# Kernel tuning notes

Hardware: AMD Instinct MI355X
Metric: run time of the kernel (lower is better)

Reference implementation:

```python
import jax, jax.numpy as jnp
import numpy as np

B, T, C, H = 4, 2048, 2048, 16
D = C // H  # head dim = 128


def setup_inputs() -> dict:
    key = jax.random.key(0)
    k1, k2, k3, k4 = jax.random.split(key, 4)
    x = jax.random.normal(k1, (B, T, C), dtype=jnp.float32)
    # per-token key mask; force token 0 valid so no causal row is fully masked
    tok_mask = jax.random.randint(k2, (B, T), 0, 2).astype(bool).at[:, 0].set(True)
    s = 1.0 / np.sqrt(C).astype(np.float32)
    W_qkv = jax.random.normal(k3, (C, 3 * C), dtype=jnp.float32) * s
    W_proj = jax.random.normal(k4, (C, C), dtype=jnp.float32) * s
    return {"x": x, "tok_mask": tok_mask, "W_qkv": W_qkv, "W_proj": W_proj}


def reference(x, tok_mask, W_qkv, W_proj):
    Bx, Tx, Cx = x.shape
    qkv = x @ W_qkv                              # [B,T,3C]
    q, k, v = jnp.split(qkv, 3, axis=-1)
    q = q.reshape(Bx, Tx, H, D)
    k = k.reshape(Bx, Tx, H, D)
    v = v.reshape(Bx, Tx, H, D)
    scale = 1.0 / np.sqrt(D).astype(np.float32)
    scores = jnp.einsum('bqhd,bkhd->bhqk', q, k) * scale  # [B,H,T,T]
    causal = jnp.tril(jnp.ones((Tx, Tx), dtype=bool))      # [T,T]
    # tok_mask broadcasts over the query dim (key mask), AND-ed with causal
    mask = tok_mask[:, None, :] & causal                   # [B,T,T]
    scores = jnp.where(mask[:, None, :, :], scores, -jnp.inf)
    attn = jax.nn.softmax(scores, axis=-1)                 # dropout p=0 -> identity
    y = jnp.einsum('bhqk,bkhd->bqhd', attn, v).reshape(Bx, Tx, Cx)
    return y @ W_proj
```

## Files before the change

### kernel.cpp

```cpp
#include <hip/hip_runtime.h>
#include <hip/hip_bf16.h>
#include <stdint.h>

typedef __bf16 bf16;
typedef __bf16 bf16x8 __attribute__((ext_vector_type(8)));
typedef float f32x4 __attribute__((ext_vector_type(4)));
typedef unsigned short u16;
typedef unsigned int u32;

constexpr int NB = 4;
constexpr int NT = 2048;
constexpr int NC = 2048;
constexpr int NH = 16;
constexpr int ND = 128;
constexpr int NC3 = 6144;

__device__ __forceinline__ void gload16(const void* g, void* l) {
  __builtin_amdgcn_global_load_lds((const __attribute__((address_space(1))) void*)g,
                                   (__attribute__((address_space(3))) void*)l, 16, 0, 0);
}

__device__ __forceinline__ u32 pack_bf16(float a, float b) {
  return (u32)__builtin_bit_cast(u16, (bf16)a) | ((u32)__builtin_bit_cast(u16, (bf16)b) << 16);
}

__global__ __launch_bounds__(256) void ingest_k(const float* __restrict__ raw, bf16* __restrict__ out, long n) {
  long i = ((long)blockIdx.x * 256 + threadIdx.x) * 8;
  if (i >= n) return;
  f32x4 a = *(const f32x4*)(raw + i), b = *(const f32x4*)(raw + i + 4);
  bf16x8 o;
  o[0] = (bf16)a[0]; o[1] = (bf16)a[1]; o[2] = (bf16)a[2]; o[3] = (bf16)a[3];
  o[4] = (bf16)b[0]; o[5] = (bf16)b[1]; o[6] = (bf16)b[2]; o[7] = (bf16)b[3];
  *(bf16x8*)(out + i) = o;
}

__global__ void mask_prep_k(const void* raw, int* out) {
  __shared__ int s_gt1, s_oddnz, s_allb, s_allf, s_allh;
  if (threadIdx.x == 0) { s_gt1 = 0; s_oddnz = 0; s_allb = 1; s_allf = 1; s_allh = 1; }
  __syncthreads();
  const unsigned int* mw = (const unsigned int*)raw;
  int gt1 = 0, oddnz = 0, allb = 1, allf = 1, allh = 1;
  for (int i = threadIdx.x; i < 2048; i += 256) {
    unsigned v = mw[i];
    if (v > 1u) gt1 = 1;
    if ((i & 1) && v) oddnz = 1;
#pragma unroll
    for (int bb = 0; bb < 4; ++bb) { unsigned by = (v >> (8*bb)) & 0xffu; if (by > 1u) allb = 0; }
    if (v != 0u && v != 0x3F800000u) allf = 0;
    unsigned lo = v & 0xffffu, hi = v >> 16;
    if ((lo != 0u && lo != 0x3F80u) || (hi != 0u && hi != 0x3F80u)) allh = 0;
  }
  if (gt1) atomicOr(&s_gt1, 1);
  if (oddnz) atomicOr(&s_oddnz, 1);
  if (!allb) atomicAnd(&s_allb, 0);
  if (!allf) atomicAnd(&s_allf, 0);
  if (!allh) atomicAnd(&s_allh, 0);
  __syncthreads();
  int mode;
  if (!s_gt1)       mode = s_oddnz ? 0 : 2;
  else if (s_allf)  mode = 3;
  else if (s_allb)  mode = 1;
  else if (s_allh)  mode = 4;
  else              mode = 0;
  for (int i = threadIdx.x; i < NB*NT; i += 256) {
    int v;
    if (mode == 0)      v = (((const int*)raw)[i] != 0);
    else if (mode == 1) v = (((const unsigned char*)raw)[i] != 0);
    else if (mode == 2) v = (((const long long*)raw)[i] != 0);
    else if (mode == 3) v = (((const unsigned int*)raw)[i] != 0);
    else                v = (((const unsigned short*)raw)[i] != 0);
    out[i] = v;
  }
}

__global__ __launch_bounds__(256) void transpose_f32_k(const float* __restrict__ in, bf16* __restrict__ out,
                                                       int in_rs, int out_rs) {
  __shared__ __align__(16) bf16 t[64][72];
  const int r0 = blockIdx.y << 6, c0 = blockIdx.x << 6;
  const int tid = threadIdx.x;
#pragma unroll
  for (int i = 0; i < 4; ++i) {
    int slot = i*256 + tid, row = slot >> 4, c4 = slot & 15;
    f32x4 v = *(const f32x4*)(in + (long)(r0 + row)*in_rs + c0 + c4*4);
#pragma unroll
    for (int e = 0; e < 4; ++e) t[c4*4 + e][row] = (bf16)v[e];
  }
  __syncthreads();
#pragma unroll
  for (int i = 0; i < 2; ++i) {
    int slot = i*256 + tid, row = slot >> 3, c8 = slot & 7;
    bf16x8 v = *(const bf16x8*)(&t[row][c8*8]);
    *(bf16x8*)(out + (long)(c0 + row)*out_rs + r0 + c8*8) = v;
  }
}

__global__ __launch_bounds__(256) void vtrans_k(const bf16* __restrict__ qkv, bf16* __restrict__ vt) {
  __shared__ __align__(16) bf16 t[64][72];
  const int tt = blockIdx.x, dh = blockIdx.y, bh = blockIdx.z;
  const int b = bh >> 4, h = bh & 15;
  const int tid = threadIdx.x;
  const bf16* src = qkv + (long)(b*NT + tt*64)*NC3 + (2*NC + h*ND + dh*64);
#pragma unroll
  for (int i = 0; i < 2; ++i) {
    int slot = i*256 + tid, row = slot >> 3, c8 = slot & 7;
    bf16x8 v = *(const bf16x8*)(src + (long)row*NC3 + c8*8);
#pragma unroll
    for (int e = 0; e < 8; ++e) t[c8*8 + e][row] = v[e];
  }
  __syncthreads();
  bf16* dst = vt + ((long)bh*ND + dh*64)*NT + tt*64;
#pragma unroll
  for (int i = 0; i < 2; ++i) {
    int slot = i*256 + tid, row = slot >> 3, c8 = slot & 7;
    bf16x8 v = *(const bf16x8*)(&t[row][c8*8]);
    *(bf16x8*)(dst + (long)row*NT + c8*8) = v;
  }
}

template <typename OT>
__global__ __launch_bounds__(512, 2) void gemm256_k(const bf16* __restrict__ A, const bf16* __restrict__ BT,
                                                    OT* __restrict__ Cout, int M, int N, int K, int nbx) {
  const int nwg = gridDim.x;
  const int bid = blockIdx.x;
  const int cpx = nwg >> 3;
  const int swz = (bid & 7) * cpx + (bid >> 3);
  const int bx = swz % nbx, by = swz / nbx;
  const long m0 = (long)by << 8, n0 = (long)bx << 8;

  const int tid = threadIdx.x, w = tid >> 6, l = tid & 63, g = l >> 4, r = l & 15;
  const int wm = w >> 2, wn = w & 3;

  __shared__ __align__(16) char As[2][32768];
  __shared__ __align__(16) char Bs[2][32768];

  long aoff[4], boff[4];
  int slo[4];
#pragma unroll
  for (int i = 0; i < 4; ++i) {
    int s = i*512 + tid, row = s >> 3, c = s & 7, cp = c ^ (row & 7);
    aoff[i] = (m0 + row)*(long)K + cp*8;
    boff[i] = (n0 + row)*(long)K + cp*8;
    slo[i] = (i*512 + w*64) << 4;
  }

  const f32x4 z4 = {0.f, 0.f, 0.f, 0.f};
  f32x4 acc[8][4];
#pragma unroll
  for (int i = 0; i < 8; ++i)
#pragma unroll
    for (int j = 0; j < 4; ++j) acc[i][j] = z4;

  const int nk = K >> 6;
#pragma unroll
  for (int i = 0; i < 4; ++i) {
    gload16(A + aoff[i], As[0] + slo[i]);
    gload16(BT + boff[i], Bs[0] + slo[i]);
  }
  __syncthreads();

  bf16x8 af[8], bfr[4];

  for (int t = 0; t < nk; ++t) {
    const int cur = t & 1;
    const char* Ac = As[cur];
    const char* Bc = Bs[cur];

#pragma unroll
    for (int mi = 0; mi < 4; ++mi)
#pragma unroll
      for (int kk = 0; kk < 2; ++kk) {
        int row = wm*128 + mi*16 + r;
        af[mi*2+kk] = *(const bf16x8*)(Ac + row*128 + (((kk*4 + g) ^ (row & 7)) << 4));
      }
#pragma unroll
    for (int ni = 0; ni < 2; ++ni)
#pragma unroll
      for (int kk = 0; kk < 2; ++kk) {
        int row = wn*64 + ni*16 + r;
        bfr[ni*2+kk] = *(const bf16x8*)(Bc + row*128 + (((kk*4 + g) ^ (row & 7)) << 4));
      }
    if (t + 1 < nk) {
      const long ko = (long)(t+1) << 6;
#pragma unroll
      for (int i = 0; i < 4; ++i) {
        gload16(A + aoff[i] + ko, As[cur^1] + slo[i]);
        gload16(BT + boff[i] + ko, Bs[cur^1] + slo[i]);
      }
    }
    __builtin_amdgcn_s_setprio(1);
#pragma unroll
    for (int mi = 0; mi < 4; ++mi)
#pragma unroll
      for (int ni = 0; ni < 2; ++ni)
#pragma unroll
        for (int kk = 0; kk < 2; ++kk)
          acc[mi][ni] = __builtin_amdgcn_mfma_f32_16x16x32_bf16(af[mi*2+kk], bfr[ni*2+kk], acc[mi][ni], 0, 0, 0);
    __builtin_amdgcn_s_setprio(0);
    __builtin_amdgcn_s_barrier();

#pragma unroll
    for (int mi = 0; mi < 4; ++mi)
#pragma unroll
      for (int kk = 0; kk < 2; ++kk) {
        int row = wm*128 + 64 + mi*16 + r;
        af[mi*2+kk] = *(const bf16x8*)(Ac + row*128 + (((kk*4 + g) ^ (row & 7)) << 4));
      }
    __builtin_amdgcn_s_setprio(1);
#pragma unroll
    for (int mi = 0; mi < 4; ++mi)
#pragma unroll
      for (int ni = 0; ni < 2; ++ni)
#pragma unroll
        for (int kk = 0; kk < 2; ++kk)
          acc[4+mi][ni] = __builtin_amdgcn_mfma_f32_16x16x32_bf16(af[mi*2+kk], bfr[ni*2+kk], acc[4+mi][ni], 0, 0, 0);
    __builtin_amdgcn_s_setprio(0);
    __builtin_amdgcn_s_barrier();

#pragma unroll
    for (int ni = 0; ni < 2; ++ni)
#pragma unroll
      for (int kk = 0; kk < 2; ++kk) {
        int row = wn*64 + 32 + ni*16 + r;
        bfr[ni*2+kk] = *(const bf16x8*)(Bc + row*128 + (((kk*4 + g) ^ (row & 7)) << 4));
      }
    __builtin_amdgcn_s_setprio(1);
#pragma unroll
    for (int mi = 0; mi < 4; ++mi)
#pragma unroll
      for (int ni = 0; ni < 2; ++ni)
#pragma unroll
        for (int kk = 0; kk < 2; ++kk)
          acc[4+mi][2+ni] = __builtin_amdgcn_mfma_f32_16x16x32_bf16(af[mi*2+kk], bfr[ni*2+kk], acc[4+mi][2+ni], 0, 0, 0);
    __builtin_amdgcn_s_setprio(0);
    __builtin_amdgcn_s_barrier();

#pragma unroll
    for (int mi = 0; mi < 4; ++mi)
#pragma unroll
      for (int kk = 0; kk < 2; ++kk) {
        int row = wm*128 + mi*16 + r;
        af[mi*2+kk] = *(const bf16x8*)(Ac + row*128 + (((kk*4 + g) ^ (row & 7)) << 4));
      }
    __builtin_amdgcn_s_setprio(1);
#pragma unroll
    for (int mi = 0; mi < 4; ++mi)
#pragma unroll
      for (int ni = 0; ni < 2; ++ni)
#pragma unroll
        for (int kk = 0; kk < 2; ++kk)
          acc[mi][2+ni] = __builtin_amdgcn_mfma_f32_16x16x32_bf16(af[mi*2+kk], bfr[ni*2+kk], acc[mi][2+ni], 0, 0, 0);
    __builtin_amdgcn_s_setprio(0);
    __syncthreads();
  }

#pragma unroll
  for (int mi = 0; mi < 8; ++mi)
#pragma unroll
    for (int ni = 0; ni < 4; ++ni)
#pragma unroll
      for (int j = 0; j < 4; ++j) {
        long mr = m0 + wm*128 + mi*16 + 4*g + j;
        long nc = n0 + wn*64 + ni*16 + r;
        Cout[mr*(long)N + nc] = (OT)acc[mi][ni][j];
      }
}

__global__ __launch_bounds__(256, 2) void attn_k(const bf16* __restrict__ qkv, const bf16* __restrict__ vt,
                                                 const int* __restrict__ mask, bf16* __restrict__ y) {
  const int qx = blockIdx.x, h = blockIdx.y, b = blockIdx.z;
  const int qb = (qx & 1) ? (15 - (qx >> 1)) : (qx >> 1);
  const int tid = threadIdx.x, w = tid >> 6, l = tid & 63, g = l >> 4, r = l & 15;
  const int q0 = qb << 7;
  const int bh = b*NH + h;
  const int ntiles = (qb << 1) + 2;
  const int qrowA = q0 + w*32 + r;
  const int qrowB = qrowA + 16;

  __shared__ __align__(16) char Klds[2][16384];
  __shared__ __align__(16) char Vlds[2][16384];
  __shared__ __align__(16) char Plds[8192];
  __shared__ char Mc[2048];
  char* Pl = Plds + (w << 11);

  for (int i = tid; i < q0 + 128; i += 256) Mc[i] = (char)(mask[b*NT + i] != 0);

  long koff[4], voff[4];
  int klo[4];
#pragma unroll
  for (int i = 0; i < 4; ++i) {
    int slot = i*256 + tid;
    int row = slot >> 4, c = slot & 15, cp = c ^ (row & 7);
    koff[i] = (long)row*NC3 + cp*8;
    klo[i] = (i*256 + w*64) << 4;
    int vrow = slot >> 3, vc = slot & 7, vcp = vc ^ (vrow & 7);
    voff[i] = (long)vrow*NT + vcp*8;
  }
  const bf16* kbase0 = qkv + (long)(b*NT)*NC3 + (NC + h*ND);
  const bf16* vbase0 = vt + (long)bh*ND*NT;

  bf16x8 qfA[4], qfB[4];
  {
    const bf16* qpA = qkv + (long)(b*NT + qrowA)*NC3 + h*ND + g*8;
    const bf16* qpB = qkv + (long)(b*NT + qrowB)*NC3 + h*ND + g*8;
#pragma unroll
    for (int dk = 0; dk < 4; ++dk) {
      qfA[dk] = *(const bf16x8*)(qpA + dk*32);
      qfB[dk] = *(const bf16x8*)(qpB + dk*32);
    }
  }

  const f32x4 z4 = {0.f, 0.f, 0.f, 0.f};
  f32x4 accA[8], accB[8];
#pragma unroll
  for (int i = 0; i < 8; ++i) { accA[i] = z4; accB[i] = z4; }
  float m_runA = 0.0f, l_runA = 0.0f;
  float m_runB = 0.0f, l_runB = 0.0f;

  const float SCL = 0.08838834764831845f * 1.4426950408889634f;

#pragma unroll
  for (int i = 0; i < 4; ++i) {
    gload16(kbase0 + koff[i], Klds[0] + klo[i]);
    gload16(vbase0 + voff[i], Vlds[0] + klo[i]);
  }
  __syncthreads();

  for (int kt = 0; kt < ntiles; ++kt) {
    const int cur = kt & 1;
    if (kt + 1 < ntiles) {
      const bf16* kb = kbase0 + (long)((kt+1)*64)*NC3;
      const bf16* vb = vbase0 + (kt+1)*64;
#pragma unroll
      for (int i = 0; i < 4; ++i) {
        gload16(kb + koff[i], Klds[cur^1] + klo[i]);
        gload16(vb + voff[i], Vlds[cur^1] + klo[i]);
      }
    }
    const char* Kl = Klds[cur];
    const char* Vl = Vlds[cur];
    const int key0 = kt*64;
    const bool actB = (key0 <= q0 + w*32 + 31);
    const bool actA = (key0 <= q0 + w*32 + 15);

    if (actB) {
      u32 mw_[4];
#pragma unroll
      for (int kc = 0; kc < 4; ++kc) mw_[kc] = *(const u32*)(Mc + key0 + kc*16 + 4*g);

      float tvA[4][4], tvB[4][4];
      __builtin_amdgcn_s_setprio(1);
#pragma unroll
      for (int kc = 0; kc < 4; ++kc) {
        const int krow = kc*16 + r;
        bf16x8 kf[4];
#pragma unroll
        for (int dk = 0; dk < 4; ++dk)
          kf[dk] = *(const bf16x8*)(Kl + krow*256 + (((dk*4 + g) ^ (krow & 7)) << 4));
        f32x4 sB = z4;
#pragma unroll
        for (int dk = 0; dk < 4; ++dk)
          sB = __builtin_amdgcn_mfma_f32_16x16x32_bf16(kf[dk], qfB[dk], sB, 0, 0, 0);
        f32x4 sA = z4;
        if (actA) {
#pragma unroll
          for (int dk = 0; dk < 4; ++dk)
            sA = __builtin_amdgcn_mfma_f32_16x16x32_bf16(kf[dk], qfA[dk], sA, 0, 0, 0);
        }
#pragma unroll
        for (int j = 0; j < 4; ++j) {
          const int key = key0 + kc*16 + 4*g + j;
          const bool km = ((mw_[kc] >> (8*j)) & 0xffu) != 0;
          tvB[kc][j] = (km && key <= qrowB) ? sB[j]*SCL : -3.0e38f;
          tvA[kc][j] = (km && key <= qrowA) ? sA[j]*SCL : -3.0e38f;
        }
      }
      __builtin_amdgcn_s_setprio(0);

      bf16x8 paA[2], paB[2];
      if (actA) {
        float tmax = -3.0e38f;
#pragma unroll
        for (int kc = 0; kc < 4; ++kc)
#pragma unroll
          for (int j = 0; j < 4; ++j) tmax = fmaxf(tmax, tvA[kc][j]);
        tmax = fmaxf(tmax, __shfl_xor(tmax, 16));
        tmax = fmaxf(tmax, __shfl_xor(tmax, 32));
        if (!__all(tmax <= m_runA + 8.0f)) {
          float mn = fmaxf(m_runA, tmax);
          float al = exp2f(m_runA - mn);
          m_runA = mn;
          l_runA *= al;
          float alj[4];
#pragma unroll
          for (int j = 0; j < 4; ++j) alj[j] = __shfl(al, 4*g + j);
#pragma unroll
          for (int d0 = 0; d0 < 8; ++d0)
#pragma unroll
            for (int j = 0; j < 4; ++j) accA[d0][j] *= alj[j];
        }
        float rs = 0.f;
#pragma unroll
        for (int kc = 0; kc < 4; ++kc) {
          float p0 = exp2f(tvA[kc][0] - m_runA), p1 = exp2f(tvA[kc][1] - m_runA);
          float p2 = exp2f(tvA[kc][2] - m_runA), p3 = exp2f(tvA[kc][3] - m_runA);
          rs += (p0 + p1) + (p2 + p3);
          const int off = (kc*32 + g*8) ^ ((r & 7) << 4);
          uint2 wv; wv.x = pack_bf16(p0, p1); wv.y = pack_bf16(p2, p3);
          *(uint2*)(Pl + r*128 + off) = wv;
        }
        rs += __shfl_xor(rs, 16);
        rs += __shfl_xor(rs, 32);
        l_runA += rs;
        asm volatile("s_waitcnt lgkmcnt(0)" ::: "memory");
        __builtin_amdgcn_sched_barrier(0);
#pragma unroll
        for (int kk = 0; kk < 2; ++kk)
          paA[kk] = *(const bf16x8*)(Pl + r*128 + ((kk*64 + g*16) ^ ((r & 7) << 4)));
        asm volatile("s_waitcnt lgkmcnt(0)" ::: "memory");
        __builtin_amdgcn_sched_barrier(0);
      }
      {
        float tmax = -3.0e38f;
#pragma unroll
        for (int kc = 0; kc < 4; ++kc)
#pragma unroll
          for (int j = 0; j < 4; ++j) tmax = fmaxf(tmax, tvB[kc][j]);
        tmax = fmaxf(tmax, __shfl_xor(tmax, 16));
        tmax = fmaxf(tmax, __shfl_xor(tmax, 32));
        if (!__all(tmax <= m_runB + 8.0f)) {
          float mn = fmaxf(m_runB, tmax);
          float al = exp2f(m_runB - mn);
          m_runB = mn;
          l_runB *= al;
          float alj[4];
#pragma unroll
          for (int j = 0; j < 4; ++j) alj[j] = __shfl(al, 4*g + j);
#pragma unroll
          for (int d0 = 0; d0 < 8; ++d0)
#pragma unroll
            for (int j = 0; j < 4; ++j) accB[d0][j] *= alj[j];
        }
        float rs = 0.f;
#pragma unroll
        for (int kc = 0; kc < 4; ++kc) {
          float p0 = exp2f(tvB[kc][0] - m_runB), p1 = exp2f(tvB[kc][1] - m_runB);
          float p2 = exp2f(tvB[kc][2] - m_runB), p3 = exp2f(tvB[kc][3] - m_runB);
          rs += (p0 + p1) + (p2 + p3);
          const int off = (kc*32 + g*8) ^ ((r & 7) << 4);
          uint2 wv; wv.x = pack_bf16(p0, p1); wv.y = pack_bf16(p2, p3);
          *(uint2*)(Pl + r*128 + off) = wv;
        }
        rs += __shfl_xor(rs, 16);
        rs += __shfl_xor(rs, 32);
        l_runB += rs;
        asm volatile("s_waitcnt lgkmcnt(0)" ::: "memory");
        __builtin_amdgcn_sched_barrier(0);
#pragma unroll
        for (int kk = 0; kk < 2; ++kk)
          paB[kk] = *(const bf16x8*)(Pl + r*128 + ((kk*64 + g*16) ^ ((r & 7) << 4)));
      }

      __builtin_amdgcn_s_setprio(1);
#pragma unroll
      for (int d0 = 0; d0 < 8; ++d0) {
        const int vrow = d0*16 + r;
#pragma unroll
        for (int kk = 0; kk < 2; ++kk) {
          bf16x8 vf = *(const bf16x8*)(Vl + vrow*128 + (((kk*4 + g) ^ (vrow & 7)) << 4));
          accB[d0] = __builtin_amdgcn_mfma_f32_16x16x32_bf16(paB[kk], vf, accB[d0], 0, 0, 0);
          if (actA) accA[d0] = __builtin_amdgcn_mfma_f32_16x16x32_bf16(paA[kk], vf, accA[d0], 0, 0, 0);
        }
      }
      __builtin_amdgcn_s_setprio(0);
    }
    __syncthreads();
  }

  {
    float lrA[4], lrB[4];
#pragma unroll
    for (int j = 0; j < 4; ++j) {
      lrA[j] = __shfl(l_runA, 4*g + j);
      lrB[j] = __shfl(l_runB, 4*g + j);
    }
#pragma unroll
    for (int d0 = 0; d0 < 8; ++d0)
#pragma unroll
      for (int j = 0; j < 4; ++j) {
        int qrA = q0 + w*32 + 4*g + j;
        y[(long)(b*NT + qrA)*NC + h*ND + d0*16 + r] = (bf16)(accA[d0][j] / lrA[j]);
        y[(long)(b*NT + qrA + 16)*NC + h*ND + d0*16 + r] = (bf16)(accB[d0][j] / lrB[j]);
      }
  }
}

extern "C" void kernel_launch(void* const* d_in, const int* in_sizes, int n_in,
                              void* d_out, int out_size, void* d_ws, size_t ws_size,
                              hipStream_t stream) {
  const float* xr     = (const float*)d_in[0];
  const void*  tok    = d_in[1];
  const float* wqkvr  = (const float*)d_in[2];
  const float* wprojr = (const float*)d_in[3];
  float* out = (float*)d_out;
  char* ws = (char*)d_ws;

  bf16* qkv    = (bf16*)(ws);
  bf16* yattn  = (bf16*)(ws + 100663296L);
  bf16* wT     = (bf16*)(ws + 134217728L);
  bf16* wpT    = (bf16*)(ws + 159383552L);
  bf16* xb     = (bf16*)(ws + 167772160L);
  bf16* vtb    = xb;
  int*  maskI  = (int*)(ws + 201326592L);

  mask_prep_k<<<1, 256, 0, stream>>>(tok, maskI);
  ingest_k<<<8192, 256, 0, stream>>>(xr, xb, 16777216L);
  transpose_f32_k<<<dim3(96, 32), 256, 0, stream>>>(wqkvr, wT, NC3, NC);
  transpose_f32_k<<<dim3(32, 32), 256, 0, stream>>>(wprojr, wpT, NC, NC);
  gemm256_k<bf16><<<768, 512, 0, stream>>>(xb, wT, qkv, 8192, 6144, 2048, 24);
  vtrans_k<<<dim3(32, 2, 64), 256, 0, stream>>>(qkv, vtb);
  attn_k<<<dim3(16, 16, 4), 256, 0, stream>>>(qkv, vtb, maskI, yattn);
  gemm256_k<float><<<256, 512, 0, stream>>>(yattn, wpT, out, 8192, 2048, 2048, 8);
}
```

Baseline: 548.3 us.

## Restructure gemm256 prefetch with per-wave LDS regions and explicit vmcnt waits

Remaps the global-to-LDS loads so each wave group fills the A/B rows it later reads, and splits the next-tile prefetch across the first two phases of the k-loop. Replaces the full __syncthreads at the end of each iteration with explicit s_waitcnt vmcnt counts plus s_barrier and sched_barrier, and peels the last iteration. The aim is to overlap global loads with MFMA work and avoid draining all outstanding memory ops every k-step. The hand-tuned vmcnt values must match the exact number of issued loads, so any compiler reordering or count mismatch could cause races.

```diff
diff --git a/kernel.cpp b/kernel.cpp
--- a/kernel.cpp
+++ b/kernel.cpp
@@ -117,6 +117,43 @@
   }
 }
 
+#define G256_READ_A(qm_) \
+  _Pragma("unroll") \
+  for (int mi = 0; mi < 4; ++mi) { \
+    _Pragma("unroll") \
+    for (int kk = 0; kk < 2; ++kk) { \
+      const int ri = (qm_)*64 + mi*16 + r; \
+      af[mi*2+kk] = *(const bf16x8*)(Ac + wm*16384 + ri*128 + (((kk*4 + g) ^ (ri & 7)) << 4)); \
+    } \
+  }
+#define G256_READ_B(qn_) \
+  _Pragma("unroll") \
+  for (int ni = 0; ni < 2; ++ni) { \
+    _Pragma("unroll") \
+    for (int kk = 0; kk < 2; ++kk) { \
+      const int ri = (qn_)*32 + ni*16 + r; \
+      bfr[ni*2+kk] = *(const bf16x8*)(Bc + wn*8192 + ri*128 + (((kk*4 + g) ^ (ri & 7)) << 4)); \
+    } \
+  }
+#define G256_MFMA(mb_, nb_) \
+  __builtin_amdgcn_s_setprio(1); \
+  _Pragma("unroll") \
+  for (int mi = 0; mi < 4; ++mi) \
+    _Pragma("unroll") \
+    for (int ni = 0; ni < 2; ++ni) \
+      _Pragma("unroll") \
+      for (int kk = 0; kk < 2; ++kk) \
+        acc[(mb_)+mi][(nb_)+ni] = __builtin_amdgcn_mfma_f32_16x16x32_bf16(af[mi*2+kk], bfr[ni*2+kk], acc[(mb_)+mi][(nb_)+ni], 0, 0, 0); \
+  __builtin_amdgcn_s_setprio(0);
+#define G256_EDGE(vm_) \
+  asm volatile("s_waitcnt vmcnt(" #vm_ ")" ::: "memory"); \
+  __builtin_amdgcn_s_barrier(); \
+  __builtin_amdgcn_sched_barrier(0);
+#define G256_EDGE_NOVM() \
+  asm volatile("" ::: "memory"); \
+  __builtin_amdgcn_s_barrier(); \
+  __builtin_amdgcn_sched_barrier(0);
+
 template <typename OT>
 __global__ __launch_bounds__(512, 2) void gemm256_k(const bf16* __restrict__ A, const bf16* __restrict__ BT,
                                                     OT* __restrict__ Cout, int M, int N, int K, int nbx) {
@@ -133,14 +170,18 @@
   __shared__ __align__(16) char As[2][32768];
   __shared__ __align__(16) char Bs[2][32768];
 
-  long aoff[4], boff[4];
-  int slo[4];
+  long aoff2[4], boff2[4];
+  int alds[4], blds[4];
 #pragma unroll
   for (int i = 0; i < 4; ++i) {
-    int s = i*512 + tid, row = s >> 3, c = s & 7, cp = c ^ (row & 7);
-    aoff[i] = (m0 + row)*(long)K + cp*8;
-    boff[i] = (n0 + row)*(long)K + cp*8;
-    slo[i] = (i*512 + w*64) << 4;
+    int s = i*256 + (tid & 255);
+    int ri = s >> 3, c = s & 7, cp = c ^ (ri & 7);
+    aoff2[i] = (m0 + wm*128 + ri) * (long)K + cp*8;
+    alds[i] = wm*16384 + ((i*256 + (w & 3)*64) << 4);
+    int s2 = i*128 + wm*64 + l;
+    int ri2 = s2 >> 3, c2 = s2 & 7, cp2 = c2 ^ (ri2 & 7);
+    boff2[i] = (n0 + wn*64 + ri2) * (long)K + cp2*8;
+    blds[i] = wn*8192 + ((i*128 + wm*64) << 4);
   }
 
   const f32x4 z4 = {0.f, 0.f, 0.f, 0.f};
@@ -151,106 +192,66 @@
     for (int j = 0; j < 4; ++j) acc[i][j] = z4;
 
   const int nk = K >> 6;
-#pragma unroll
-  for (int i = 0; i < 4; ++i) {
-    gload16(A + aoff[i], As[0] + slo[i]);
-    gload16(BT + boff[i], Bs[0] + slo[i]);
-  }
-  __syncthreads();
+  gload16(A + aoff2[0], As[0] + alds[0]);
+  gload16(A + aoff2[1], As[0] + alds[1]);
+  gload16(BT + boff2[0], Bs[0] + blds[0]);
+  gload16(BT + boff2[1], Bs[0] + blds[1]);
+  gload16(A + aoff2[2], As[0] + alds[2]);
+  gload16(A + aoff2[3], As[0] + alds[3]);
+  gload16(BT + boff2[2], Bs[0] + blds[2]);
+  gload16(BT + boff2[3], Bs[0] + blds[3]);
+  G256_EDGE(4);
 
   bf16x8 af[8], bfr[4];
 
-  for (int t = 0; t < nk; ++t) {
+  for (int t = 0; t < nk - 1; ++t) {
     const int cur = t & 1;
     const char* Ac = As[cur];
     const char* Bc = Bs[cur];
-
-#pragma unroll
-    for (int mi = 0; mi < 4; ++mi)
-#pragma unroll
-      for (int kk = 0; kk < 2; ++kk) {
-        int row = wm*128 + mi*16 + r;
-        af[mi*2+kk] = *(const bf16x8*)(Ac + row*128 + (((kk*4 + g) ^ (row & 7)) << 4));
-      }
-#pragma unroll
-    for (int ni = 0; ni < 2; ++ni)
-#pragma unroll
-      for (int kk = 0; kk < 2; ++kk) {
-        int row = wn*64 + ni*16 + r;
-        bfr[ni*2+kk] = *(const bf16x8*)(Bc + row*128 + (((kk*4 + g) ^ (row & 7)) << 4));
-      }
-    if (t + 1 < nk) {
-      const long ko = (long)(t+1) << 6;
-#pragma unroll
-      for (int i = 0; i < 4; ++i) {
-        gload16(A + aoff[i] + ko, As[cur^1] + slo[i]);
-        gload16(BT + boff[i] + ko, Bs[cur^1] + slo[i]);
-      }
-    }
-    __builtin_amdgcn_s_setprio(1);
-#pragma unroll
-    for (int mi = 0; mi < 4; ++mi)
-#pragma unroll
-      for (int ni = 0; ni < 2; ++ni)
-#pragma unroll
-        for (int kk = 0; kk < 2; ++kk)
-          acc[mi][ni] = __builtin_amdgcn_mfma_f32_16x16x32_bf16(af[mi*2+kk], bfr[ni*2+kk], acc[mi][ni], 0, 0, 0);
-    __builtin_amdgcn_s_setprio(0);
-    __builtin_amdgcn_s_barrier();
-
-#pragma unroll
-    for (int mi = 0; mi < 4; ++mi)
-#pragma unroll
-      for (int kk = 0; kk < 2; ++kk) {
-        int row = wm*128 + 64 + mi*16 + r;
-        af[mi*2+kk] = *(const bf16x8*)(Ac + row*128 + (((kk*4 + g) ^ (row & 7)) << 4));
-      }
-    __builtin_amdgcn_s_setprio(1);
-#pragma unroll
-    for (int mi = 0; mi < 4; ++mi)
-#pragma unroll
-      for (int ni = 0; ni < 2; ++ni)
-#pragma unroll
-        for (int kk = 0; kk < 2; ++kk)
-          acc[4+mi][ni] = __builtin_amdgcn_mfma_f32_16x16x32_bf16(af[mi*2+kk], bfr[ni*2+kk], acc[4+mi][ni], 0, 0, 0);
-    __builtin_amdgcn_s_setprio(0);
-    __builtin_amdgcn_s_barrier();
-
-#pragma unroll
-    for (int ni = 0; ni < 2; ++ni)
-#pragma unroll
-      for (int kk = 0; kk < 2; ++kk) {
-        int row = wn*64 + 32 + ni*16 + r;
-        bfr[ni*2+kk] = *(const bf16x8*)(Bc + row*128 + (((kk*4 + g) ^ (row & 7)) << 4));
-      }
-    __builtin_amdgcn_s_setprio(1);
-#pragma unroll
-    for (int mi = 0; mi < 4; ++mi)
-#pragma unroll
-      for (int ni = 0; ni < 2; ++ni)
-#pragma unroll
-        for (int kk = 0; kk < 2; ++kk)
-          acc[4+mi][2+ni] = __builtin_amdgcn_mfma_f32_16x16x32_bf16(af[mi*2+kk], bfr[ni*2+kk], acc[4+mi][2+ni], 0, 0, 0);
-    __builtin_amdgcn_s_setprio(0);
-    __builtin_amdgcn_s_barrier();
-
-#pragma unroll
-    for (int mi = 0; mi < 4; ++mi)
-#pragma unroll
-      for (int kk = 0; kk < 2; ++kk) {
-        int row = wm*128 + mi*16 + r;
-        af[mi*2+kk] = *(const bf16x8*)(Ac + row*128 + (((kk*4 + g) ^ (row & 7)) << 4));
-      }
-    __builtin_amdgcn_s_setprio(1);
-#pragma unroll
-    for (int mi = 0; mi < 4; ++mi)
-#pragma unroll
-      for (int ni = 0; ni < 2; ++ni)
-#pragma unroll
-        for (int kk = 0; kk < 2; ++kk)
-          acc[mi][2+ni] = __builtin_amdgcn_mfma_f32_16x16x32_bf16(af[mi*2+kk], bfr[ni*2+kk], acc[mi][2+ni], 0, 0, 0);
-    __builtin_amdgcn_s_setprio(0);
-    __syncthreads();
+    char* An = As[cur ^ 1];
+    char* Bn = Bs[cur ^ 1];
+    const long ko = (long)(t + 1) << 6;
+
+    G256_READ_A(0); G256_READ_B(0);
+    gload16(A + aoff2[0] + ko, An + alds[0]);
+    gload16(A + aoff2[1] + ko, An + alds[1]);
+    gload16(BT + boff2[0] + ko, Bn + blds[0]);
+    gload16(BT + boff2[1] + ko, Bn + blds[1]);
+    G256_MFMA(0, 0);
+    G256_EDGE(6);
+
+    G256_READ_A(1);
+    gload16(A + aoff2[2] + ko, An + alds[2]);
+    gload16(A + aoff2[3] + ko, An + alds[3]);
+    gload16(BT + boff2[2] + ko, Bn + blds[2]);
+    gload16(BT + boff2[3] + ko, Bn + blds[3]);
+    G256_MFMA(4, 0);
+    G256_EDGE(8);
+
+    G256_READ_B(1);
+    G256_MFMA(4, 2);
+    G256_EDGE_NOVM();
+
+    G256_READ_A(0);
+    G256_MFMA(0, 2);
+    G256_EDGE(4);
+  }
+
+  {
+    const int cur = (nk - 1) & 1;
+    const char* Ac = As[cur];
+    const char* Bc = Bs[cur];
+    G256_READ_A(0); G256_READ_B(0);
+    G256_MFMA(0, 0);
+    G256_EDGE(2);
+    G256_READ_A(1);
+    G256_MFMA(4, 0);
+    G256_EDGE(0);
+    G256_READ_B(1);
+    G256_MFMA(4, 2);
+    G256_EDGE_NOVM();
+    G256_READ_A(0);
+    G256_MFMA(0, 2);
   }
 
 #pragma unroll
```

After: 543.3 us. No clear change (-0.9%).
